# Optimization experiments

Measured on AMD Instinct MI355X. Metric: run time of the kernel, lower is better.

Reference implementation:

```python
import jax, jax.numpy as jnp
import numpy as np
from jax import lax

B, T, I, H, O = 64, 2048, 128, 256, 1


def setup_inputs() -> dict:
    key = jax.random.key(0)
    ks = jax.random.split(key, 8)
    lim_ih = 1.0 / np.sqrt(H)
    inp = {
        "xd": jax.random.normal(ks[0], (B, T, I), jnp.float32),
        "w": jax.random.normal(ks[1], (B, T, I), jnp.float32),
        # eqx.nn.LSTMCell params: gates stacked [i, f, g, o] along first axis
        "W_ih": jax.random.uniform(ks[2], (4 * H, I), jnp.float32, -lim_ih, lim_ih),
        "b_ih": jax.random.uniform(ks[3], (4 * H,), jnp.float32, -lim_ih, lim_ih),
        "W_hh": jax.random.uniform(ks[4], (4 * H, H), jnp.float32, -lim_ih, lim_ih),
        "b_hh": jax.random.uniform(ks[5], (4 * H,), jnp.float32, -lim_ih, lim_ih),
        "W_out": jax.random.uniform(ks[6], (O, H), jnp.float32, -lim_ih, lim_ih),
        "b_out": jax.random.uniform(ks[7], (O,), jnp.float32, -lim_ih, lim_ih),
    }
    return inp


def reference(xd, w, W_ih, b_ih, W_hh, b_hh, W_out, b_out):
    # Input gating (elementwise), then precompute the input-to-gates GEMM for
    # the whole sequence (mathematically identical to doing it per step).
    gated = xd * jax.nn.sigmoid(w)                       # [B,T,I]
    x_part = jnp.einsum("bti,gi->btg", gated, W_ih) + b_ih  # [B,T,4H]
    x_part = jnp.swapaxes(x_part, 0, 1)                  # [T,B,4H] for scan

    def step(state, xp):
        h, c = state
        z = xp + h @ W_hh.T + b_hh                       # [B,4H]
        i, f, g, o = jnp.split(z, 4, axis=-1)            # eqx gate order i,f,g,o
        c = jax.nn.sigmoid(f) * c + jax.nn.sigmoid(i) * jnp.tanh(g)
        h = jax.nn.sigmoid(o) * jnp.tanh(c)
        return (h, c), None

    init = (jnp.zeros((B, H), xd.dtype), jnp.zeros((B, H), xd.dtype))
    (h_T, _), _ = lax.scan(step, init, x_part)
    return h_T @ W_out.T + b_out                         # [B,O]
```

## Files before the change

kernel.cpp:

```cpp
#include <hip/hip_runtime.h>
#include <hip/hip_fp16.h>
#include <stdint.h>


#define NB 64
#define NT 2048
#define NI 128
#define NH 256

typedef _Float16 h8_t __attribute__((ext_vector_type(8)));
typedef _Float16 h4_t __attribute__((ext_vector_type(4)));
typedef float f4_t __attribute__((ext_vector_type(4)));

__device__ __forceinline__ float sigm(float x) {
  return __builtin_amdgcn_rcpf(1.f + __expf(-x));
}
__device__ __forceinline__ float tanh_f(float x) {
  return 1.f - 2.f * __builtin_amdgcn_rcpf(1.f + __expf(2.f * x));
}


#define STEP(T, XV, WGV, FAST) do {                                         \
  const int tt = (T);                                                       \
  {                                                                         \
    h4_t gx;                                                                \
    gx[0] = (_Float16)(XV[0] * sigm(WGV[0]));                               \
    gx[1] = (_Float16)(XV[1] * sigm(WGV[1]));                               \
    gx[2] = (_Float16)(XV[2] * sigm(WGV[2]));                               \
    gx[3] = (_Float16)(XV[3] * sigm(WGV[3]));                               \
    *(h4_t*)(&Alds[bl][jj * 4]) = gx;                                       \
  }                                                                         \
  if (tt + 2 < NT) {       \
    XV  = *(const f4_t*)(xd + xbase + (size_t)(tt + 2) * NI);               \
    WGV = *(const f4_t*)(w  + xbase + (size_t)(tt + 2) * NI);               \
  }                                                                         \
  if (tt > 0) {                                                             \
    uint64_t* base = (FAST ? exf : exs) + ((tt & 1) << 14);                 \
    unsigned need = 0x7f;                                                   \
    uint64_t v[7];                                                          \
    while (need) {                                                          \
      _Pragma("unroll")                                                     \
      for (int s7 = 0; s7 < 7; ++s7)                                        \
        if (need & (1u << s7))                                              \
          v[s7] = FAST ? __hip_atomic_fetch_or(base + pidx[s7], z0,         \
                             __ATOMIC_RELAXED, __HIP_MEMORY_SCOPE_WORKGROUP)\
                       : __hip_atomic_load(base + pidx[s7], __ATOMIC_RELAXED,\
                             __HIP_MEMORY_SCOPE_AGENT);                     \
      _Pragma("unroll")                                                     \
      for (int s7 = 0; s7 < 7; ++s7)                                        \
        if ((need & (1u << s7)) &&                                          \
            (unsigned)(v[s7] >> 32) == (unsigned)tt) {                      \
          int ps = (s7 < p) ? s7 : s7 + 1;                                  \
          Alds[bl][NI + ps * 32 + jj] =                                     \
              (_Float16)__uint_as_float((unsigned)v[s7]);                   \
          need &= ~(1u << s7);                                              \
        }                                                                   \
    }                                                                       \
  }                                                                         \
  __syncthreads();                          \
  {                                                                         \
    f4_t acc0 = {0.f, 0.f, 0.f, 0.f}, acc1 = {0.f, 0.f, 0.f, 0.f};         \
    _Pragma("unroll")                                                       \
    for (int kt = 0; kt < 12; ++kt) {                                       \
      h8_t af = *(const h8_t*)(&Alds[cc][kt * 32 + q * 8]);                 \
      acc0 = __builtin_amdgcn_mfma_f32_16x16x32_f16(af, wf[0][kt], acc0,    \
                                                    0, 0, 0);               \
      acc1 = __builtin_amdgcn_mfma_f32_16x16x32_f16(af, wf[1][kt], acc1,    \
                                                    0, 0, 0);               \
    }                                                                       \
    if (q < 2) {                                                            \
      _Pragma("unroll")                                                     \
      for (int r = 0; r < 4; ++r) {                                         \
        Zlds[16 * (2 * wv)     + cc][q * 4 + r] = acc0[r];                  \
        Zlds[16 * (2 * wv + 1) + cc][q * 4 + r] = acc1[r];                  \
      }                                                                     \
    }                                                                       \
  }                                                                         \
  __syncthreads();                               \
  {                                                                         \
    float zi = Zlds[jj * 4 + 0][bl] + bias[0];                              \
    float zf = Zlds[jj * 4 + 1][bl] + bias[1];                              \
    float zg = Zlds[jj * 4 + 2][bl] + bias[2];                              \
    float zo = Zlds[jj * 4 + 3][bl] + bias[3];                              \
    creg = sigm(zf) * creg + sigm(zi) * tanh_f(zg);                         \
    hreg = sigm(zo) * tanh_f(creg);                                         \
    uint64_t pay =                                                          \
        ((uint64_t)(unsigned)(tt + 1) << 32) | __float_as_uint(hreg);       \
    if (FAST)                                                               \
      (void)__hip_atomic_exchange(exf + (((tt + 1) & 1) << 14) + myidx,     \
                                  pay, __ATOMIC_RELAXED,                    \
                                  __HIP_MEMORY_SCOPE_WORKGROUP);            \
    else                                                                    \
      __hip_atomic_store(exs + (((tt + 1) & 1) << 14) + myidx, pay,         \
                         __ATOMIC_RELAXED, __HIP_MEMORY_SCOPE_AGENT);       \
    Alds[bl][NI + p * 32 + jj] = (_Float16)hreg;     \
  }                                                                         \
} while (0)

__launch_bounds__(256, 1)
__global__ void lstm_persist(
    const float* __restrict__ xd, const float* __restrict__ w,
    const float* __restrict__ W_ih, const float* __restrict__ b_ih,
    const float* __restrict__ W_hh, const float* __restrict__ b_hh,
    const float* __restrict__ W_out, const float* __restrict__ b_out,
    float* __restrict__ out, uint64_t* ex, int mode)
{
  const int bid = blockIdx.x;
  const int tid = threadIdx.x;
  const int lane = tid & 63;
  const int wv = tid >> 6;
  const int q  = lane >> 4;
  const int cc = lane & 15;
  const int bl = tid >> 5;
  const int jj = tid & 31;

  __shared__ _Float16 Alds[16][392];
  __shared__ float Zlds[128][17];
  __shared__ int xcc_sh[64];
  __shared__ int meta_sh[4];
  __shared__ int m_sh[8];
  __shared__ uint64_t gen_sh;

  for (int i = tid; i < 16 * 392; i += 256) (&Alds[0][0])[i] = (_Float16)0.f;

  uint64_t z0;
  asm volatile("s_mov_b64 %0, 0" : "=s"(z0));

  uint64_t* const exf = ex;
  uint64_t* const exs = mode ? (ex + 32768) : ex;
  uint64_t* const exA = ex + 65536;
  uint64_t* const exB = ex + 65600;
  uint64_t* const exg = ex + 65664;

  int g, p, fastmode = 0;

  if (mode) {
    if (tid == 0) {
      uint64_t old = __hip_atomic_fetch_add(exg + bid, 1, __ATOMIC_RELAXED,
                                            __HIP_MEMORY_SCOPE_AGENT);
      gen_sh = (old + 1) & 0x00FFFFFFFFFFFFFFull;
    }
    __syncthreads();
    const uint64_t gen = gen_sh;

    if (tid == 0) {
      unsigned x;
      asm volatile("s_getreg_b32 %0, hwreg(HW_REG_XCC_ID)" : "=s"(x));
      __hip_atomic_store(exA + bid, (gen << 8) | (uint64_t)(x & 0xffu),
                         __ATOMIC_RELAXED, __HIP_MEMORY_SCOPE_AGENT);
    }
    if (tid < 64) {
      uint64_t e;
      do {
        e = __hip_atomic_load(exA + tid, __ATOMIC_RELAXED,
                              __HIP_MEMORY_SCOPE_AGENT);
      } while ((e >> 8) != gen);
      xcc_sh[tid] = (int)(e & 0xff);
    }
    __syncthreads();

    if (tid == 0) {
      const int myx = xcc_sh[bid];
      int bal = 1;
      for (int b = 0; b < 64; ++b) {
        int c = 0;
        for (int b2 = 0; b2 < 64; ++b2) c += (xcc_sh[b2] == xcc_sh[b]);
        if (c != 8) { bal = 0; break; }
      }
      int gd = 0, rank = 0, mi = 0;
      for (int b = 0; b < 64; ++b) {
        if (xcc_sh[b] == myx) {
          if (b < bid) rank++;
          if (mi < 8) m_sh[mi++] = b;
        } else if (xcc_sh[b] < myx) {
          bool first = true;
          for (int b2 = 0; b2 < b; ++b2)
            if (xcc_sh[b2] == xcc_sh[b]) { first = false; break; }
          gd += first;
        }
      }
      meta_sh[0] = bal; meta_sh[1] = gd; meta_sh[2] = rank;
    }
    __syncthreads();
    const int bal = meta_sh[0];
    if (bal) { g = meta_sh[1]; p = meta_sh[2]; }
    else     { g = bid & 7;    p = bid >> 3;   }

    if (bal) {
      const int myidx_p = g * 2048 + p * 256 + bl * 32 + jj;
      int pidx_p[7];
      #pragma unroll
      for (int s7 = 0; s7 < 7; ++s7) {
        int ps = (s7 < p) ? s7 : s7 + 1;
        pidx_p[s7] = g * 2048 + ps * 256 + bl * 32 + jj;
      }
      const unsigned ptag = 0x7E000000u | ((unsigned)gen & 0xFFFFFFu);
      (void)__hip_atomic_exchange(
          exf + myidx_p, ((uint64_t)ptag << 32) | (unsigned)bid,
          __ATOMIC_RELAXED, __HIP_MEMORY_SCOPE_WORKGROUP);
      unsigned need = 0x7f;
      for (int sw = 0; sw < 400 && need; ++sw) {
        uint64_t v[7];
        #pragma unroll
        for (int s7 = 0; s7 < 7; ++s7)
          if (need & (1u << s7))
            v[s7] = __hip_atomic_fetch_or(exf + pidx_p[s7], z0,
                                          __ATOMIC_RELAXED,
                                          __HIP_MEMORY_SCOPE_WORKGROUP);
        #pragma unroll
        for (int s7 = 0; s7 < 7; ++s7)
          if ((need & (1u << s7)) && (unsigned)(v[s7] >> 32) == ptag)
            need &= ~(1u << s7);
      }
      int allok = __syncthreads_and(need == 0);
      if (tid == 0) {
        __hip_atomic_store(exB + bid,
                           (gen << 8) | 0x40ull | (uint64_t)(allok ? 1 : 0),
                           __ATOMIC_RELAXED, __HIP_MEMORY_SCOPE_AGENT);
        int fm = 1;
        for (int k = 0; k < 8; ++k) {
          uint64_t vv;
          do {
            vv = __hip_atomic_load(exB + m_sh[k], __ATOMIC_RELAXED,
                                   __HIP_MEMORY_SCOPE_AGENT);
          } while ((vv >> 8) != gen);
          fm &= (int)(vv & 1u);
        }
        meta_sh[3] = fm;
      }
      __syncthreads();
      fastmode = meta_sh[3];
    }
  } else {
    g = bid & 7;
    p = bid >> 3;
  }

  h8_t wf[2][12];
  for (int nt = 0; nt < 2; ++nt) {
    int r = 16 * (2 * wv + nt) + cc;
    int R = (r & 3) * NH + p * 32 + (r >> 2);
    for (int kt = 0; kt < 12; ++kt) {
      int k = kt * 32 + q * 8;
      const float* s = (k < NI) ? (W_ih + (size_t)R * NI + k)
                                : (W_hh + (size_t)R * NH + (k - NI));
      f4_t lo = *(const f4_t*)s;
      f4_t hi = *(const f4_t*)(s + 4);
      h8_t hh;
      hh[0] = (_Float16)lo[0]; hh[1] = (_Float16)lo[1];
      hh[2] = (_Float16)lo[2]; hh[3] = (_Float16)lo[3];
      hh[4] = (_Float16)hi[0]; hh[5] = (_Float16)hi[1];
      hh[6] = (_Float16)hi[2]; hh[7] = (_Float16)hi[3];
      wf[nt][kt] = hh;
    }
  }

  float bias[4];
  #pragma unroll
  for (int gate = 0; gate < 4; ++gate)
    bias[gate] = b_ih[gate * NH + p * 32 + jj] + b_hh[gate * NH + p * 32 + jj];

  int pidx[7];
  #pragma unroll
  for (int s7 = 0; s7 < 7; ++s7) {
    int ps = (s7 < p) ? s7 : s7 + 1;
    pidx[s7] = g * 2048 + ps * 256 + bl * 32 + jj;
  }
  const int myidx = g * 2048 + p * 256 + bl * 32 + jj;

  float creg = 0.f;
  float hreg = 0.f;
  const size_t xbase = ((size_t)(g * 8 + bl) * NT) * NI + jj * 4;

  f4_t xvA = *(const f4_t*)(xd + xbase);
  f4_t wgA = *(const f4_t*)(w  + xbase);
  f4_t xvB = *(const f4_t*)(xd + xbase + NI);
  f4_t wgB = *(const f4_t*)(w  + xbase + NI);

  __syncthreads();

  if (fastmode) {
    for (int t = 0; t < NT; t += 2) {
      STEP(t,     xvA, wgA, 1);
      STEP(t + 1, xvB, wgB, 1);
    }
  } else {
    for (int t = 0; t < NT; t += 2) {
      STEP(t,     xvA, wgA, 0);
      STEP(t + 1, xvB, wgB, 0);
    }
  }

  if (p == 0) {
    float sum = hreg * W_out[jj];
    unsigned need = 0x7f;
    float hv[7];
    uint64_t v[7];
    while (need) {
      #pragma unroll
      for (int s7 = 0; s7 < 7; ++s7)
        if (need & (1u << s7))
          v[s7] = fastmode
                      ? __hip_atomic_fetch_or(exf + pidx[s7], z0,
                                              __ATOMIC_RELAXED,
                                              __HIP_MEMORY_SCOPE_WORKGROUP)
                      : __hip_atomic_load(exs + pidx[s7], __ATOMIC_RELAXED,
                                          __HIP_MEMORY_SCOPE_AGENT);
      #pragma unroll
      for (int s7 = 0; s7 < 7; ++s7)
        if ((need & (1u << s7)) && (unsigned)(v[s7] >> 32) == (unsigned)NT) {
          hv[s7] = __uint_as_float((unsigned)v[s7]);
          need &= ~(1u << s7);
        }
    }
    #pragma unroll
    for (int s7 = 0; s7 < 7; ++s7) {
      int ps = (s7 < p) ? s7 : s7 + 1;
      sum += hv[s7] * W_out[ps * 32 + jj];
    }
    #pragma unroll
    for (int m = 16; m >= 1; m >>= 1) sum += __shfl_xor(sum, m, 64);
    if (jj == 0) out[g * 8 + bl] = sum + b_out[0];
  }
}

extern "C" void kernel_launch(void* const* d_in, const int* in_sizes, int n_in,
                              void* d_out, int out_size, void* d_ws, size_t ws_size,
                              hipStream_t stream) {
  (void)in_sizes; (void)n_in; (void)out_size;
  const float* xd    = (const float*)d_in[0];
  const float* w     = (const float*)d_in[1];
  const float* W_ih  = (const float*)d_in[2];
  const float* b_ih  = (const float*)d_in[3];
  const float* W_hh  = (const float*)d_in[4];
  const float* b_hh  = (const float*)d_in[5];
  const float* W_out = (const float*)d_in[6];
  const float* b_out = (const float*)d_in[7];
  uint64_t* ex = (uint64_t*)d_ws;
  const size_t NEEDED = (size_t)65728 * 8;
  int mode = (ws_size >= NEEDED) ? 1 : 0;
  lstm_persist<<<dim3(64), dim3(256), 0, stream>>>(
      xd, w, W_ih, b_ih, W_hh, b_hh, W_out, b_out, (float*)d_out, ex, mode);
}
```

Measured before the change: 3.729 ms.

## Pack h exchange into half2 payloads, add per-block flags, overlap input MFMA with polling

```diff
diff --git a/kernel.cpp b/kernel.cpp
--- a/kernel.cpp
+++ b/kernel.cpp
@@ -20,63 +20,87 @@
 }
 
 
-#define STEP(T, XV, WGV, FAST) do {                                         \
+#define DATARND(DB, TG32, S) do {                                           \
+  uint64_t v[7];                                                            \
+  _Pragma("unroll")                                                         \
+  for (int s7 = 0; s7 < 7; ++s7)                                            \
+    if (need & (1u << s7))                                                  \
+      v[s7] = __hip_atomic_fetch_or((DB) + didx[s7], z0,                    \
+                                    __ATOMIC_RELAXED, S);                   \
+  _Pragma("unroll")                                                         \
+  for (int s7 = 0; s7 < 7; ++s7)                                            \
+    if ((need & (1u << s7)) && (unsigned)(v[s7] >> 32) == (TG32)) {         \
+      int ps = (s7 < p) ? s7 : s7 + 1;                                      \
+      *(unsigned*)(&HLDS[bl][ps * 32 + 2 * jj]) = (unsigned)v[s7];          \
+      need &= ~(1u << s7);                                                  \
+    }                                                                       \
+} while (0)
+
+#define STEP(T, XVC, WGC, XVN, WGN, S) do {                                 \
   const int tt = (T);                                                       \
+  if (tt + 2 < NT) {      \
+    XVC = *(const f4_t*)(xd + xbase + (size_t)(tt + 2) * NI);               \
+    WGC = *(const f4_t*)(w  + xbase + (size_t)(tt + 2) * NI);               \
+  }                                                                         \
+  \
+  f4_t acc0 = {0.f, 0.f, 0.f, 0.f}, acc1 = {0.f, 0.f, 0.f, 0.f};           \
   {                                                                         \
-    h4_t gx;                                                                \
-    gx[0] = (_Float16)(XV[0] * sigm(WGV[0]));                               \
-    gx[1] = (_Float16)(XV[1] * sigm(WGV[1]));                               \
-    gx[2] = (_Float16)(XV[2] * sigm(WGV[2]));                               \
-    gx[3] = (_Float16)(XV[3] * sigm(WGV[3]));                               \
-    *(h4_t*)(&Alds[bl][jj * 4]) = gx;                                       \
-  }                                                                         \
-  if (tt + 2 < NT) {       \
-    XV  = *(const f4_t*)(xd + xbase + (size_t)(tt + 2) * NI);               \
-    WGV = *(const f4_t*)(w  + xbase + (size_t)(tt + 2) * NI);               \
-  }                                                                         \
-  if (tt > 0) {                                                             \
-    uint64_t* base = (FAST ? exf : exs) + ((tt & 1) << 14);                 \
-    unsigned need = 0x7f;                                                   \
-    uint64_t v[7];                                                          \
-    while (need) {                                                          \
-      _Pragma("unroll")                                                     \
-      for (int s7 = 0; s7 < 7; ++s7)                                        \
-        if (need & (1u << s7))                                              \
-          v[s7] = FAST ? __hip_atomic_fetch_or(base + pidx[s7], z0,         \
-                             __ATOMIC_RELAXED, __HIP_MEMORY_SCOPE_WORKGROUP)\
-                       : __hip_atomic_load(base + pidx[s7], __ATOMIC_RELAXED,\
-                             __HIP_MEMORY_SCOPE_AGENT);                     \
-      _Pragma("unroll")                                                     \
-      for (int s7 = 0; s7 < 7; ++s7)                                        \
-        if ((need & (1u << s7)) &&                                          \
-            (unsigned)(v[s7] >> 32) == (unsigned)tt) {                      \
-          int ps = (s7 < p) ? s7 : s7 + 1;                                  \
-          Alds[bl][NI + ps * 32 + jj] =                                     \
-              (_Float16)__uint_as_float((unsigned)v[s7]);                   \
-          need &= ~(1u << s7);                                              \
-        }                                                                   \
-    }                                                                       \
-  }                                                                         \
-  __syncthreads();                          \
-  {                                                                         \
-    f4_t acc0 = {0.f, 0.f, 0.f, 0.f}, acc1 = {0.f, 0.f, 0.f, 0.f};         \
+    const _Float16* xb = &XLDS[tt & 1][0][0];                               \
     _Pragma("unroll")                                                       \
-    for (int kt = 0; kt < 12; ++kt) {                                       \
-      h8_t af = *(const h8_t*)(&Alds[cc][kt * 32 + q * 8]);                 \
+    for (int kt = 0; kt < 4; ++kt) {                                        \
+      h8_t af = *(const h8_t*)(xb + cc * 136 + kt * 32 + q * 8);            \
       acc0 = __builtin_amdgcn_mfma_f32_16x16x32_f16(af, wf[0][kt], acc0,    \
                                                     0, 0, 0);               \
       acc1 = __builtin_amdgcn_mfma_f32_16x16x32_f16(af, wf[1][kt], acc1,    \
                                                     0, 0, 0);               \
     }                                                                       \
-    if (q < 2) {                                                            \
-      _Pragma("unroll")                                                     \
-      for (int r = 0; r < 4; ++r) {                                         \
-        Zlds[16 * (2 * wv)     + cc][q * 4 + r] = acc0[r];                  \
-        Zlds[16 * (2 * wv + 1) + cc][q * 4 + r] = acc1[r];                  \
+  }                                                                         \
+         \
+  if (tt > 0) {                                                             \
+    const uint64_t tgt = (gen << 12) | (uint64_t)tt;                        \
+    const unsigned tg32 = (unsigned)tgt;                                    \
+    uint64_t* db = DAT + ((tt & 1) << 13);                                  \
+    unsigned need = (jj < 16) ? 0x7fu : 0u;                                 \
+    if (need) DATARND(db, tg32, S);      \
+    if (__ballot(need != 0)) {                                              \
+      for (;;) {                         \
+        uint64_t fv = 0;                                                    \
+        if (lane < 7)                                                       \
+          fv = __hip_atomic_fetch_or(FLG + fidx_l, z0,                      \
+                                     __ATOMIC_RELAXED, S);                  \
+        if (__ballot((lane < 7) ? (fv >= tgt) : 1) == ~0ull) break;         \
       }                                                                     \
+      while (need) DATARND(db, tg32, S);                                    \
+    }                                                                       \
+  }                                                                         \
+  __syncthreads();                          \
+    \
+  if (tt + 1 < NT) {                                                        \
+    h4_t gx;                                                                \
+    gx[0] = (_Float16)(XVN[0] * sigm(WGN[0]));                              \
+    gx[1] = (_Float16)(XVN[1] * sigm(WGN[1]));                              \
+    gx[2] = (_Float16)(XVN[2] * sigm(WGN[2]));                              \
+    gx[3] = (_Float16)(XVN[3] * sigm(WGN[3]));                              \
+    *(h4_t*)(&XLDS[(tt + 1) & 1][bl][jj * 4]) = gx;                         \
+  }                                                                         \
+                                 \
+  _Pragma("unroll")                                                         \
+  for (int kt = 4; kt < 12; ++kt) {                                         \
+    h8_t af = *(const h8_t*)(&HLDS[cc][(kt - 4) * 32 + q * 8]);             \
+    acc0 = __builtin_amdgcn_mfma_f32_16x16x32_f16(af, wf[0][kt], acc0,      \
+                                                  0, 0, 0);                 \
+    acc1 = __builtin_amdgcn_mfma_f32_16x16x32_f16(af, wf[1][kt], acc1,      \
+                                                  0, 0, 0);                 \
+  }                                                                         \
+  if (q < 2) {                                                              \
+    _Pragma("unroll")                                                       \
+    for (int r = 0; r < 4; ++r) {                                           \
+      Zlds[16 * (2 * wv)     + cc][q * 4 + r] = acc0[r];                    \
+      Zlds[16 * (2 * wv + 1) + cc][q * 4 + r] = acc1[r];                    \
     }                                                                       \
   }                                                                         \
   __syncthreads();                               \
+               \
   {                                                                         \
     float zi = Zlds[jj * 4 + 0][bl] + bias[0];                              \
     float zf = Zlds[jj * 4 + 1][bl] + bias[1];                              \
@@ -84,16 +108,22 @@
     float zo = Zlds[jj * 4 + 3][bl] + bias[3];                              \
     creg = sigm(zf) * creg + sigm(zi) * tanh_f(zg);                         \
     hreg = sigm(zo) * tanh_f(creg);                                         \
-    uint64_t pay =                                                          \
-        ((uint64_t)(unsigned)(tt + 1) << 32) | __float_as_uint(hreg);       \
-    if (FAST)                                                               \
-      (void)__hip_atomic_exchange(exf + (((tt + 1) & 1) << 14) + myidx,     \
-                                  pay, __ATOMIC_RELAXED,                    \
-                                  __HIP_MEMORY_SCOPE_WORKGROUP);            \
-    else                                                                    \
-      __hip_atomic_store(exs + (((tt + 1) & 1) << 14) + myidx, pay,         \
-                         __ATOMIC_RELAXED, __HIP_MEMORY_SCOPE_AGENT);       \
-    Alds[bl][NI + p * 32 + jj] = (_Float16)hreg;     \
+    HLDS[bl][p * 32 + jj] = (_Float16)hreg;          \
+    float h0 = __shfl(hreg, slA, 64);                 \
+    float h1 = __shfl(hreg, slA + 1, 64);                                   \
+    if (jj < 16) {                                                          \
+      _Float16 a0 = (_Float16)h0, a1 = (_Float16)h1;                        \
+      unsigned h01 = (unsigned)*(unsigned short*)&a0 |                      \
+                     ((unsigned)*(unsigned short*)&a1 << 16);               \
+      unsigned tagp = (unsigned)((gen << 12) | (uint64_t)(tt + 1));         \
+      uint64_t pay = ((uint64_t)tagp << 32) | h01;                          \
+      (void)__hip_atomic_exchange(DAT + (((tt + 1) & 1) << 13) + dmy, pay,  \
+                                  __ATOMIC_RELAXED, S);                     \
+    }                                                                       \
+    if (tid == 0)                                                           \
+      (void)__hip_atomic_exchange(FLG + fown,                               \
+                                  (gen << 12) | (uint64_t)(tt + 1),         \
+                                  __ATOMIC_RELAXED, S);                     \
   }                                                                         \
 } while (0)
 
@@ -114,45 +144,46 @@
   const int bl = tid >> 5;
   const int jj = tid & 31;
 
-  __shared__ _Float16 Alds[16][392];
+  __shared__ _Float16 XLDS[2][16][136];
+  __shared__ _Float16 HLDS[16][264];
   __shared__ float Zlds[128][17];
   __shared__ int xcc_sh[64];
-  __shared__ int meta_sh[4];
-  __shared__ int m_sh[8];
+  __shared__ int meta_sh[3];
   __shared__ uint64_t gen_sh;
 
-  for (int i = tid; i < 16 * 392; i += 256) (&Alds[0][0])[i] = (_Float16)0.f;
+  for (int i = tid; i < 2 * 16 * 136; i += 256) (&XLDS[0][0][0])[i] = (_Float16)0.f;
+  for (int i = tid; i < 16 * 264;     i += 256) (&HLDS[0][0])[i]    = (_Float16)0.f;
 
   uint64_t z0;
   asm volatile("s_mov_b64 %0, 0" : "=s"(z0));
 
-  uint64_t* const exf = ex;
-  uint64_t* const exs = mode ? (ex + 32768) : ex;
-  uint64_t* const exA = ex + 65536;
-  uint64_t* const exB = ex + 65600;
-  uint64_t* const exg = ex + 65664;
-
-  int g, p, fastmode = 0;
+  uint64_t* const DAT = ex;
+  uint64_t* const FLG = ex + 16384;
+  uint64_t* const XCC = ex + 16896;
+  uint64_t* const GEN = ex + 16960;
+
+  int g, p, bal = 0;
+  uint64_t gen = 1;
 
   if (mode) {
     if (tid == 0) {
-      uint64_t old = __hip_atomic_fetch_add(exg + bid, 1, __ATOMIC_RELAXED,
+      uint64_t old = __hip_atomic_fetch_add(GEN + bid, 1, __ATOMIC_RELAXED,
                                             __HIP_MEMORY_SCOPE_AGENT);
       gen_sh = (old + 1) & 0x00FFFFFFFFFFFFFFull;
     }
     __syncthreads();
-    const uint64_t gen = gen_sh;
+    gen = gen_sh;
 
     if (tid == 0) {
       unsigned x;
       asm volatile("s_getreg_b32 %0, hwreg(HW_REG_XCC_ID)" : "=s"(x));
-      __hip_atomic_store(exA + bid, (gen << 8) | (uint64_t)(x & 0xffu),
+      __hip_atomic_store(XCC + bid, (gen << 8) | (uint64_t)(x & 0xffu),
                          __ATOMIC_RELAXED, __HIP_MEMORY_SCOPE_AGENT);
     }
     if (tid < 64) {
       uint64_t e;
       do {
-        e = __hip_atomic_load(exA + tid, __ATOMIC_RELAXED,
+        e = __hip_atomic_load(XCC + tid, __ATOMIC_RELAXED,
                               __HIP_MEMORY_SCOPE_AGENT);
       } while ((e >> 8) != gen);
       xcc_sh[tid] = (int)(e & 0xff);
@@ -161,17 +192,16 @@
 
     if (tid == 0) {
       const int myx = xcc_sh[bid];
-      int bal = 1;
+      int balL = 1;
       for (int b = 0; b < 64; ++b) {
         int c = 0;
         for (int b2 = 0; b2 < 64; ++b2) c += (xcc_sh[b2] == xcc_sh[b]);
-        if (c != 8) { bal = 0; break; }
+        if (c != 8) { balL = 0; break; }
       }
-      int gd = 0, rank = 0, mi = 0;
+      int gd = 0, rank = 0;
       for (int b = 0; b < 64; ++b) {
         if (xcc_sh[b] == myx) {
           if (b < bid) rank++;
-          if (mi < 8) m_sh[mi++] = b;
         } else if (xcc_sh[b] < myx) {
           bool first = true;
           for (int b2 = 0; b2 < b; ++b2)
@@ -179,58 +209,12 @@
           gd += first;
         }
       }
-      meta_sh[0] = bal; meta_sh[1] = gd; meta_sh[2] = rank;
+      meta_sh[0] = balL; meta_sh[1] = gd; meta_sh[2] = rank;
     }
     __syncthreads();
-    const int bal = meta_sh[0];
+    bal = meta_sh[0];
     if (bal) { g = meta_sh[1]; p = meta_sh[2]; }
     else     { g = bid & 7;    p = bid >> 3;   }
-
-    if (bal) {
-      const int myidx_p = g * 2048 + p * 256 + bl * 32 + jj;
-      int pidx_p[7];
-      #pragma unroll
-      for (int s7 = 0; s7 < 7; ++s7) {
-        int ps = (s7 < p) ? s7 : s7 + 1;
-        pidx_p[s7] = g * 2048 + ps * 256 + bl * 32 + jj;
-      }
-      const unsigned ptag = 0x7E000000u | ((unsigned)gen & 0xFFFFFFu);
-      (void)__hip_atomic_exchange(
-          exf + myidx_p, ((uint64_t)ptag << 32) | (unsigned)bid,
-          __ATOMIC_RELAXED, __HIP_MEMORY_SCOPE_WORKGROUP);
-      unsigned need = 0x7f;
-      for (int sw = 0; sw < 400 && need; ++sw) {
-        uint64_t v[7];
-        #pragma unroll
-        for (int s7 = 0; s7 < 7; ++s7)
-          if (need & (1u << s7))
-            v[s7] = __hip_atomic_fetch_or(exf + pidx_p[s7], z0,
-                                          __ATOMIC_RELAXED,
-                                          __HIP_MEMORY_SCOPE_WORKGROUP);
-        #pragma unroll
-        for (int s7 = 0; s7 < 7; ++s7)
-          if ((need & (1u << s7)) && (unsigned)(v[s7] >> 32) == ptag)
-            need &= ~(1u << s7);
-      }
-      int allok = __syncthreads_and(need == 0);
-      if (tid == 0) {
-        __hip_atomic_store(exB + bid,
-                           (gen << 8) | 0x40ull | (uint64_t)(allok ? 1 : 0),
-                           __ATOMIC_RELAXED, __HIP_MEMORY_SCOPE_AGENT);
-        int fm = 1;
-        for (int k = 0; k < 8; ++k) {
-          uint64_t vv;
-          do {
-            vv = __hip_atomic_load(exB + m_sh[k], __ATOMIC_RELAXED,
-                                   __HIP_MEMORY_SCOPE_AGENT);
-          } while ((vv >> 8) != gen);
-          fm &= (int)(vv & 1u);
-        }
-        meta_sh[3] = fm;
-      }
-      __syncthreads();
-      fastmode = meta_sh[3];
-    }
   } else {
     g = bid & 7;
     p = bid >> 3;
@@ -260,13 +244,18 @@
   for (int gate = 0; gate < 4; ++gate)
     bias[gate] = b_ih[gate * NH + p * 32 + jj] + b_hh[gate * NH + p * 32 + jj];
 
-  int pidx[7];
+  int didx[7];
   #pragma unroll
   for (int s7 = 0; s7 < 7; ++s7) {
     int ps = (s7 < p) ? s7 : s7 + 1;
-    pidx[s7] = g * 2048 + ps * 256 + bl * 32 + jj;
-  }
-  const int myidx = g * 2048 + p * 256 + bl * 32 + jj;
+    didx[s7] = (g * 8 + ps) * 128 + bl * 16 + jj;
+  }
+  const int s7l = (lane < 7) ? lane : 0;
+  const int psl = (s7l < p) ? s7l : s7l + 1;
+  const int fidx_l = (g * 8 + psl) * 8;
+  const int fown = (g * 8 + p) * 8;
+  const int dmy = (g * 8 + p) * 128 + bl * 16 + jj;
+  const int slA = (bl & 1) * 32 + 2 * jj;
 
   float creg = 0.f;
   float hreg = 0.f;
@@ -274,50 +263,57 @@
 
   f4_t xvA = *(const f4_t*)(xd + xbase);
   f4_t wgA = *(const f4_t*)(w  + xbase);
+  {
+    h4_t gx;
+    gx[0] = (_Float16)(xvA[0] * sigm(wgA[0]));
+    gx[1] = (_Float16)(xvA[1] * sigm(wgA[1]));
+    gx[2] = (_Float16)(xvA[2] * sigm(wgA[2]));
+    gx[3] = (_Float16)(xvA[3] * sigm(wgA[3]));
+    *(h4_t*)(&XLDS[0][bl][jj * 4]) = gx;
+  }
   f4_t xvB = *(const f4_t*)(xd + xbase + NI);
   f4_t wgB = *(const f4_t*)(w  + xbase + NI);
 
   __syncthreads();
 
-  if (fastmode) {
+  if (bal) {
     for (int t = 0; t < NT; t += 2) {
-      STEP(t,     xvA, wgA, 1);
-      STEP(t + 1, xvB, wgB, 1);
+      STEP(t,     xvA, wgA, xvB, wgB, __HIP_MEMORY_SCOPE_WORKGROUP);
+      STEP(t + 1, xvB, wgB, xvA, wgA, __HIP_MEMORY_SCOPE_WORKGROUP);
     }
   } else {
     for (int t = 0; t < NT; t += 2) {
-      STEP(t,     xvA, wgA, 0);
-      STEP(t + 1, xvB, wgB, 0);
+      STEP(t,     xvA, wgA, xvB, wgB, __HIP_MEMORY_SCOPE_AGENT);
+      STEP(t + 1, xvB, wgB, xvA, wgA, __HIP_MEMORY_SCOPE_AGENT);
     }
   }
 
   if (p == 0) {
-    float sum = hreg * W_out[jj];
-    unsigned need = 0x7f;
-    float hv[7];
-    uint64_t v[7];
-    while (need) {
-      #pragma unroll
-      for (int s7 = 0; s7 < 7; ++s7)
-        if (need & (1u << s7))
-          v[s7] = fastmode
-                      ? __hip_atomic_fetch_or(exf + pidx[s7], z0,
-                                              __ATOMIC_RELAXED,
-                                              __HIP_MEMORY_SCOPE_WORKGROUP)
-                      : __hip_atomic_load(exs + pidx[s7], __ATOMIC_RELAXED,
-                                          __HIP_MEMORY_SCOPE_AGENT);
-      #pragma unroll
-      for (int s7 = 0; s7 < 7; ++s7)
-        if ((need & (1u << s7)) && (unsigned)(v[s7] >> 32) == (unsigned)NT) {
-          hv[s7] = __uint_as_float((unsigned)v[s7]);
-          need &= ~(1u << s7);
-        }
-    }
+    const uint64_t tgt = (gen << 12) | (uint64_t)NT;
+    const unsigned tg32 = (unsigned)tgt;
+    uint64_t* db = DAT;
+    unsigned need = (jj < 16) ? 0x7fu : 0u;
+    if (need) DATARND(db, tg32,
+                      bal ? __HIP_MEMORY_SCOPE_WORKGROUP
+                          : __HIP_MEMORY_SCOPE_AGENT);
+    if (__ballot(need != 0)) {
+      for (;;) {
+        uint64_t fv = 0;
+        if (lane < 7)
+          fv = __hip_atomic_fetch_or(FLG + fidx_l, z0, __ATOMIC_RELAXED,
+                                     bal ? __HIP_MEMORY_SCOPE_WORKGROUP
+                                         : __HIP_MEMORY_SCOPE_AGENT);
+        if (__ballot((lane < 7) ? (fv >= tgt) : 1) == ~0ull) break;
+      }
+      while (need) DATARND(db, tg32,
+                           bal ? __HIP_MEMORY_SCOPE_WORKGROUP
+                               : __HIP_MEMORY_SCOPE_AGENT);
+    }
+    __syncthreads();
+    float sum = 0.f;
     #pragma unroll
-    for (int s7 = 0; s7 < 7; ++s7) {
-      int ps = (s7 < p) ? s7 : s7 + 1;
-      sum += hv[s7] * W_out[ps * 32 + jj];
-    }
+    for (int s = 0; s < 8; ++s)
+      sum += (float)HLDS[bl][s * 32 + jj] * W_out[s * 32 + jj];
     #pragma unroll
     for (int m = 16; m >= 1; m >>= 1) sum += __shfl_xor(sum, m, 64);
     if (jj == 0) out[g * 8 + bl] = sum + b_out[0];
@@ -337,7 +333,7 @@
   const float* W_out = (const float*)d_in[6];
   const float* b_out = (const float*)d_in[7];
   uint64_t* ex = (uint64_t*)d_ws;
-  const size_t NEEDED = (size_t)65728 * 8;
+  const size_t NEEDED = (size_t)17024 * 8;
   int mode = (ws_size >= NEEDED) ? 1 : 0;
   lstm_persist<<<dim3(64), dim3(256), 0, stream>>>(
       xd, w, W_ih, b_ih, W_hh, b_hh, W_out, b_out, (float*)d_out, ex, mode);
```

Measured after the change: 4.864 ms. +30.4%, slower.
